# Kernel optimization log

Measured on AMD Instinct MI355X. Metric: run time of the kernel, lower is better.

The kernel has to match this reference:

```python
import jax, jax.numpy as jnp
import numpy as np

N_TOKEN = 1024
N_I = 512
VOCAB = 10
D = 1024
L = 12
H_MLP = 4096
EPS = 1e-5  # torch LayerNorm default
B = 8


def layer_norm(x, g, b):
    mu = jnp.mean(x, axis=-1, keepdims=True)
    var = jnp.mean(jnp.square(x - mu), axis=-1, keepdims=True)
    return (x - mu) * jax.lax.rsqrt(var + EPS) * g + b


def setup_inputs() -> dict:
    key = jax.random.key(0)
    ks = jax.random.split(key, 12)
    s = 0.02  # init scale for weights
    return {
        'xt': jax.random.randint(ks[0], (B, N_TOKEN - N_I), 0, VOCAB),
        'zi': jax.random.randint(ks[1], (B, N_I), 0, VOCAB),
        'pos_emb': jax.random.normal(ks[2], (N_TOKEN, D), jnp.float32) * s,
        't_emb': jax.random.normal(ks[3], (VOCAB, D), jnp.float32) * s,
        'Wq': jax.random.normal(ks[4], (L, D, D), jnp.float32) * s,
        'Wk': jax.random.normal(ks[5], (L, D, D), jnp.float32) * s,
        'Wv': jax.random.normal(ks[6], (L, D, D), jnp.float32) * s,
        'ln1_g': jnp.ones((L, D), jnp.float32),
        'ln1_b': jnp.zeros((L, D), jnp.float32),
        'ln2_g': jnp.ones((L, D), jnp.float32),
        'ln2_b': jnp.zeros((L, D), jnp.float32),
        'mlp_w1': jax.random.normal(ks[7], (L, D, H_MLP), jnp.float32) * s,
        'mlp_b1': jnp.zeros((L, H_MLP), jnp.float32),
        'mlp_w2': jax.random.normal(ks[8], (L, H_MLP, D), jnp.float32) * s,
        'mlp_b2': jnp.zeros((L, D), jnp.float32),
        'ro_w': jax.random.normal(ks[9], (D, 1), jnp.float32) * s,
        'ro_b': jnp.zeros((1,), jnp.float32),
    }


def _forward(xt, zi, pos_emb, t_emb, Wq, Wk, Wv, ln1_g, ln1_b, ln2_g, ln2_b,
             mlp_w1, mlp_b1, mlp_w2, mlp_b2, ro_w, ro_b):
    # token embeddings: image tokens get -(c - zi)^2/2 in the first VOCAB dims, 0 elsewhere
    opts = jnp.arange(VOCAB, dtype=jnp.float32)
    leave = -jnp.square(opts[None, None, :] - zi[:, :, None].astype(jnp.float32)) * 0.5  # [B, N_I, V]
    emb_i = jnp.pad(leave, ((0, 0), (0, 0), (0, D - VOCAB)))  # [B, N_I, D]
    emb_t = t_emb[xt]                                          # [B, T1, D]
    H = jnp.concatenate([emb_i, emb_t], axis=1) + pos_emb[None, :, :]  # [B, T, D]

    inv_sqrt_d = np.float32(1.0 / np.sqrt(D))

    def step(H, p):
        wq, wk, wv, g1, b1, g2, b2, w1, bb1, w2, bb2 = p
        H1 = layer_norm(H, g1, b1)
        q = H1 @ wq
        k = H1 @ wk
        v = H1 @ wv
        attn = jnp.einsum('bid,bjd->bij', q, k) * inv_sqrt_d  # [B, T, T]
        attn = jax.nn.softmax(attn, axis=-1)
        H = H + jnp.einsum('bij,bjd->bid', attn, v)
        H2 = layer_norm(H, g2, b2)
        # torch nn.GELU default is exact (erf) gelu
        H = H + (jax.nn.gelu(H2 @ w1 + bb1, approximate=False) @ w2 + bb2)
        return H, None

    H, _ = jax.lax.scan(step, H, (Wq, Wk, Wv, ln1_g, ln1_b, ln2_g, ln2_b,
                                  mlp_w1, mlp_b1, mlp_w2, mlp_b2))
    pred = H @ ro_w + ro_b  # [B, T, 1]
    return pred[:, :N_I, 0]  # [B, N_I]


def reference(xt, zi, pos_emb, t_emb, Wq, Wk, Wv, ln1_g, ln1_b, ln2_g, ln2_b,
              mlp_w1, mlp_b1, mlp_w2, mlp_b2, ro_w, ro_b):
    return _forward(xt, zi, pos_emb, t_emb, Wq, Wk, Wv, ln1_g, ln1_b, ln2_g, ln2_b,
                    mlp_w1, mlp_b1, mlp_w2, mlp_b2, ro_w, ro_b)
```

## Files before the change

kernel.cpp:

```cpp
#include <hip/hip_runtime.h>
#include <cstdint>
#include <cmath>

typedef unsigned short u16;
typedef unsigned int u32;
typedef short bf16x8 __attribute__((ext_vector_type(8)));
typedef float f32x4 __attribute__((ext_vector_type(4)));

#define DEV static __device__ __forceinline__

DEV u16 f2bf(float f) {
  union { float f; u32 u; } v; v.f = f;
  return (u16)((v.u + 0x7FFFu + ((v.u >> 16) & 1u)) >> 16);
}
DEV float bf2f(u32 lo16) {
  union { u32 u; float f; } v; v.u = lo16 << 16; return v.f;
}

DEV void gload16(const void* g, u16* l) {
  __builtin_amdgcn_global_load_lds(
      (const __attribute__((address_space(1))) void*)g,
      (__attribute__((address_space(3))) void*)l, 16, 0, 0);
}

template<int MODE>
__global__ __launch_bounds__(512, 4)
void gemm8(const u16* __restrict__ A, const u16* __restrict__ Bt,
           void* __restrict__ Cv, const float* __restrict__ bias,
           u16* __restrict__ Vt, int M, int N, int K, int ldA, int ldB,
           float scale)
{
  __shared__ __align__(16) u16 As[128 * 64];
  __shared__ __align__(16) u16 Bs[128 * 64];

  const long m0 = (long)blockIdx.x * 128, n0 = (long)blockIdx.y * 128;
  const int t = threadIdx.x;
  const int wave = t >> 6, lane = t & 63;
  const int wr = (wave >> 2) * 64, wc = (wave & 3) * 32;
  const int lg = lane >> 4, lr = lane & 15;

  const long ldA2 = (long)ldA * 2, ldB2 = (long)ldB * 2;

  const int rl = lane >> 3, c7 = lane & 7;
  const int sb = (c7 * 16) ^ (rl << 4);
  const char* aP[2]; const char* bP[2];
  u16* aL[2]; u16* bL[2];
  {
    const char* Ab = (const char*)A;
    const char* Bb = (const char*)Bt;
    #pragma unroll
    for (int c = 0; c < 2; ++c) {
      const int q = c * 8 + wave;
      aP[c] = Ab + (m0 + q * 8 + rl) * ldA2 + sb;
      bP[c] = Bb + (n0 + q * 8 + rl) * ldB2 + sb;
      aL[c] = As + q * 512;
      bL[c] = Bs + q * 512;
    }
  }

  const int rswz = (lr & 7) << 4;
  auto rd = [&](const u16* base, int row, int cbyte) -> bf16x8 {
    return *reinterpret_cast<const bf16x8*>(
        reinterpret_cast<const char*>(base) + row * 128 + (cbyte ^ rswz));
  };

  f32x4 acc[4][2];
  #pragma unroll
  for (int i = 0; i < 4; ++i)
    #pragma unroll
    for (int j = 0; j < 2; ++j)
      acc[i][j] = (f32x4){0.f, 0.f, 0.f, 0.f};

  for (int k0 = 0; k0 < K; k0 += 64) {
    #pragma unroll
    for (int c = 0; c < 2; ++c) {
      gload16(aP[c], aL[c]);
      gload16(bP[c], bL[c]);
      aP[c] += 128; bP[c] += 128;
    }
    __syncthreads();

    #pragma unroll
    for (int ks = 0; ks < 2; ++ks) {
      bf16x8 a[4], b[2];
      #pragma unroll
      for (int i = 0; i < 4; ++i)
        a[i] = rd(As, wr + i * 16 + lr, ks * 64 + lg * 16);
      #pragma unroll
      for (int i = 0; i < 2; ++i)
        b[i] = rd(Bs, wc + i * 16 + lr, ks * 64 + lg * 16);
      #pragma unroll
      for (int mi = 0; mi < 4; ++mi)
        #pragma unroll
        for (int ni = 0; ni < 2; ++ni)
          acc[mi][ni] = __builtin_amdgcn_mfma_f32_16x16x32_bf16(a[mi], b[ni], acc[mi][ni], 0, 0, 0);
    }
    __syncthreads();
  }

  #pragma unroll
  for (int mi = 0; mi < 4; ++mi) {
    #pragma unroll
    for (int ni = 0; ni < 2; ++ni) {
      #pragma unroll
      for (int r = 0; r < 4; ++r) {
        const long grow = m0 + wr + mi * 16 + lg * 4 + r;
        const long gcol = n0 + wc + ni * 16 + lr;
        const float v = acc[mi][ni][r];
        if constexpr (MODE == 3) {
          const float x = v + bias[gcol];
          const float u2 = 1.59576912f * x * (1.f + 0.044715f * x * x);
          const float ge = x / (1.f + __expf(-u2));
          ((u16*)Cv)[grow * N + gcol] = f2bf(ge);
        } else if constexpr (MODE == 4) {
          float* Cp = (float*)Cv;
          const long idx = grow * N + gcol;
          Cp[idx] = Cp[idx] + v + bias[gcol];
        } else if constexpr (MODE == 5) {
          if (gcol < 2048) {
            ((u16*)Cv)[grow * 2048 + gcol] = f2bf(v * scale);
          } else {
            const long b = grow >> 10, tk = grow & 1023, d = gcol - 2048;
            Vt[(b << 20) + (d << 10) + tk] = f2bf(v);
          }
        }
      }
    }
  }
}

template<int MODE>
__global__ __launch_bounds__(512, 4)
void gemm8b(const u16* __restrict__ A, const u16* __restrict__ Bt,
            void* __restrict__ Cv, int N, int K, int ldA, int ldB,
            long sA, long sB, long sC, float scale)
{
  __shared__ __align__(16) u16 As[128 * 64];
  __shared__ __align__(16) u16 Bs[128 * 64];

  const int bz = blockIdx.z;
  const long m0 = (long)blockIdx.x * 128, n0 = (long)blockIdx.y * 128;
  const int t = threadIdx.x;
  const int wave = t >> 6, lane = t & 63;
  const int wr = (wave >> 2) * 64, wc = (wave & 3) * 32;
  const int lg = lane >> 4, lr = lane & 15;

  const long ldA2 = (long)ldA * 2, ldB2 = (long)ldB * 2;

  const int rl = lane >> 3, c7 = lane & 7;
  const int sb = (c7 * 16) ^ (rl << 4);
  const char* aP[2]; const char* bP[2];
  u16* aL[2]; u16* bL[2];
  {
    const char* Ab = (const char*)(A + (long)bz * sA);
    const char* Bb = (const char*)(Bt + (long)bz * sB);
    #pragma unroll
    for (int c = 0; c < 2; ++c) {
      const int q = c * 8 + wave;
      aP[c] = Ab + (m0 + q * 8 + rl) * ldA2 + sb;
      bP[c] = Bb + (n0 + q * 8 + rl) * ldB2 + sb;
      aL[c] = As + q * 512;
      bL[c] = Bs + q * 512;
    }
  }

  const int rswz = (lr & 7) << 4;
  auto rd = [&](const u16* base, int row, int cbyte) -> bf16x8 {
    return *reinterpret_cast<const bf16x8*>(
        reinterpret_cast<const char*>(base) + row * 128 + (cbyte ^ rswz));
  };

  f32x4 acc[4][2];
  #pragma unroll
  for (int i = 0; i < 4; ++i)
    #pragma unroll
    for (int j = 0; j < 2; ++j)
      acc[i][j] = (f32x4){0.f, 0.f, 0.f, 0.f};

  for (int k0 = 0; k0 < K; k0 += 64) {
    #pragma unroll
    for (int c = 0; c < 2; ++c) {
      gload16(aP[c], aL[c]);
      gload16(bP[c], bL[c]);
      aP[c] += 128; bP[c] += 128;
    }
    __syncthreads();

    #pragma unroll
    for (int ks = 0; ks < 2; ++ks) {
      bf16x8 a[4], b[2];
      #pragma unroll
      for (int i = 0; i < 4; ++i)
        a[i] = rd(As, wr + i * 16 + lr, ks * 64 + lg * 16);
      #pragma unroll
      for (int i = 0; i < 2; ++i)
        b[i] = rd(Bs, wc + i * 16 + lr, ks * 64 + lg * 16);
      #pragma unroll
      for (int mi = 0; mi < 4; ++mi)
        #pragma unroll
        for (int ni = 0; ni < 2; ++ni)
          acc[mi][ni] = __builtin_amdgcn_mfma_f32_16x16x32_bf16(a[mi], b[ni], acc[mi][ni], 0, 0, 0);
    }
    __syncthreads();
  }

  #pragma unroll
  for (int mi = 0; mi < 4; ++mi) {
    #pragma unroll
    for (int ni = 0; ni < 2; ++ni) {
      #pragma unroll
      for (int r = 0; r < 4; ++r) {
        const long grow = m0 + wr + mi * 16 + lg * 4 + r;
        const long gcol = n0 + wc + ni * 16 + lr;
        const float v = acc[mi][ni][r];
        if constexpr (MODE == 0) {
          u16* Cp = (u16*)Cv + (long)bz * sC;
          Cp[grow * N + gcol] = f2bf(v * scale);
        } else if constexpr (MODE == 2) {
          float* Cp = (float*)Cv + (long)bz * sC;
          Cp[grow * N + gcol] += v;
        }
      }
    }
  }
}

__global__ __launch_bounds__(256)
void trans_k(const float* __restrict__ wq, const float* __restrict__ wk,
             const float* __restrict__ wv, const float* __restrict__ w1,
             const float* __restrict__ w2, u16* __restrict__ ob)
{
  __shared__ u16 T[64][68];
  const int b = blockIdx.x;
  const float* in; u16* out; int K, N, tk, tn;
  if (b < 768) {
    const int m = b >> 8, tt = b & 255;
    in = (m == 0) ? wq : (m == 1) ? wk : wv;
    out = ob + (long)m * 1048576L;
    K = 1024; N = 1024; tk = tt >> 4; tn = tt & 15;
  } else if (b < 1792) {
    const int tt = b - 768;
    in = w1; out = ob + 3L * 1048576L; K = 1024; N = 4096;
    tk = tt >> 6; tn = tt & 63;
  } else {
    const int tt = b - 1792;
    in = w2; out = ob + 7L * 1048576L; K = 4096; N = 1024;
    tk = tt >> 4; tn = tt & 15;
  }
  const int k0 = tk * 64, n0 = tn * 64;
  const int t = threadIdx.x;
  {
    const int r = t >> 2, cq = (t & 3) * 16;
    const float* src = in + (long)(k0 + r) * N + n0 + cq;
    #pragma unroll
    for (int q = 0; q < 4; ++q) {
      const float4 v = *reinterpret_cast<const float4*>(src + q * 4);
      T[r][cq + q * 4 + 0] = f2bf(v.x);
      T[r][cq + q * 4 + 1] = f2bf(v.y);
      T[r][cq + q * 4 + 2] = f2bf(v.z);
      T[r][cq + q * 4 + 3] = f2bf(v.w);
    }
  }
  __syncthreads();
  {
    const int n = t >> 2, kq2 = (t & 3) * 16;
    u16 tmp[16];
    #pragma unroll
    for (int j = 0; j < 16; ++j) tmp[j] = T[kq2 + j][n];
    uint4* dst = reinterpret_cast<uint4*>(out + (long)(n0 + n) * K + k0 + kq2);
    dst[0] = *reinterpret_cast<const uint4*>(&tmp[0]);
    dst[1] = *reinterpret_cast<const uint4*>(&tmp[8]);
  }
}

__global__ __launch_bounds__(256)
void embed_k(const int* __restrict__ xt, const int* __restrict__ zi,
             const float* __restrict__ pos, const float* __restrict__ temb,
             float* __restrict__ H)
{
  const int bt = blockIdx.x;
  const int b = bt >> 10, tk = bt & 1023;
  const int d = threadIdx.x * 4;
  const float4 p = reinterpret_cast<const float4*>(pos + (long)tk * 1024)[threadIdx.x];
  float4 v;
  if (tk < 512) {
    const float z = (float)zi[b * 512 + tk];
    const float c0 = (float)(d + 0) - z, c1 = (float)(d + 1) - z;
    const float c2 = (float)(d + 2) - z, c3 = (float)(d + 3) - z;
    v.x = (d + 0 < 10) ? -0.5f * c0 * c0 : 0.f;
    v.y = (d + 1 < 10) ? -0.5f * c1 * c1 : 0.f;
    v.z = (d + 2 < 10) ? -0.5f * c2 * c2 : 0.f;
    v.w = (d + 3 < 10) ? -0.5f * c3 * c3 : 0.f;
  } else {
    const float* te = temb + (long)xt[b * 512 + (tk - 512)] * 1024;
    v = reinterpret_cast<const float4*>(te)[threadIdx.x];
  }
  float4 o; o.x = v.x + p.x; o.y = v.y + p.y; o.z = v.z + p.z; o.w = v.w + p.w;
  reinterpret_cast<float4*>(H + (long)bt * 1024)[threadIdx.x] = o;
}

__global__ __launch_bounds__(256)
void ln_k(const float* __restrict__ X, const float* __restrict__ g,
          const float* __restrict__ bta, u16* __restrict__ Y)
{
  __shared__ float sm[8];
  const long row = blockIdx.x;
  const float4 x = reinterpret_cast<const float4*>(X + row * 1024)[threadIdx.x];
  float s1 = x.x + x.y + x.z + x.w;
  float s2 = x.x * x.x + x.y * x.y + x.z * x.z + x.w * x.w;
  #pragma unroll
  for (int o = 32; o > 0; o >>= 1) { s1 += __shfl_down(s1, o); s2 += __shfl_down(s2, o); }
  const int w = threadIdx.x >> 6, ln = threadIdx.x & 63;
  if (ln == 0) { sm[w] = s1; sm[4 + w] = s2; }
  __syncthreads();
  s1 = sm[0] + sm[1] + sm[2] + sm[3];
  s2 = sm[4] + sm[5] + sm[6] + sm[7];
  const float mu = s1 * (1.f / 1024.f);
  const float var = s2 * (1.f / 1024.f) - mu * mu;
  const float inv = rsqrtf(var + 1e-5f);
  const float4 gg = reinterpret_cast<const float4*>(g)[threadIdx.x];
  const float4 bb = reinterpret_cast<const float4*>(bta)[threadIdx.x];
  const u32 o0 = (u32)f2bf((x.x - mu) * inv * gg.x + bb.x) | ((u32)f2bf((x.y - mu) * inv * gg.y + bb.y) << 16);
  const u32 o1 = (u32)f2bf((x.z - mu) * inv * gg.z + bb.z) | ((u32)f2bf((x.w - mu) * inv * gg.w + bb.w) << 16);
  reinterpret_cast<uint2*>(Y + row * 1024)[threadIdx.x] = make_uint2(o0, o1);
}

__global__ __launch_bounds__(256)
void sm_k(const u16* __restrict__ S, u16* __restrict__ P)
{
  __shared__ float sm[8];
  const long row = blockIdx.x;
  const uint2 raw = reinterpret_cast<const uint2*>(S + row * 1024)[threadIdx.x];
  const float x0 = bf2f(raw.x & 0xffffu), x1 = bf2f(raw.x >> 16);
  const float x2 = bf2f(raw.y & 0xffffu), x3 = bf2f(raw.y >> 16);
  float m = fmaxf(fmaxf(x0, x1), fmaxf(x2, x3));
  #pragma unroll
  for (int o = 32; o > 0; o >>= 1) m = fmaxf(m, __shfl_down(m, o));
  const int w = threadIdx.x >> 6, ln = threadIdx.x & 63;
  if (ln == 0) sm[w] = m;
  __syncthreads();
  m = fmaxf(fmaxf(sm[0], sm[1]), fmaxf(sm[2], sm[3]));
  const float e0 = __expf(x0 - m), e1 = __expf(x1 - m);
  const float e2 = __expf(x2 - m), e3 = __expf(x3 - m);
  float s = e0 + e1 + e2 + e3;
  #pragma unroll
  for (int o = 32; o > 0; o >>= 1) s += __shfl_down(s, o);
  if (ln == 0) sm[4 + w] = s;
  __syncthreads();
  const float tot = sm[4] + sm[5] + sm[6] + sm[7];
  const float r = 1.0f / tot;
  const u32 o0 = (u32)f2bf(e0 * r) | ((u32)f2bf(e1 * r) << 16);
  const u32 o1 = (u32)f2bf(e2 * r) | ((u32)f2bf(e3 * r) << 16);
  reinterpret_cast<uint2*>(P + row * 1024)[threadIdx.x] = make_uint2(o0, o1);
}

__global__ __launch_bounds__(256)
void ro_k(const float* __restrict__ H, const float* __restrict__ w,
          const float* __restrict__ b, float* __restrict__ out)
{
  __shared__ float sm[4];
  const int row = blockIdx.x;
  const int bb = row >> 9, i = row & 511;
  const float* h = H + ((long)bb * 1024 + i) * 1024;
  const float4 x = reinterpret_cast<const float4*>(h)[threadIdx.x];
  const float4 ww = reinterpret_cast<const float4*>(w)[threadIdx.x];
  float s = x.x * ww.x + x.y * ww.y + x.z * ww.z + x.w * ww.w;
  #pragma unroll
  for (int o = 32; o > 0; o >>= 1) s += __shfl_down(s, o);
  const int wv = threadIdx.x >> 6, ln = threadIdx.x & 63;
  if (ln == 0) sm[wv] = s;
  __syncthreads();
  if (threadIdx.x == 0) out[row] = sm[0] + sm[1] + sm[2] + sm[3] + b[0];
}

extern "C" void kernel_launch(void* const* d_in, const int* in_sizes, int n_in,
                              void* d_out, int out_size, void* d_ws, size_t ws_size,
                              hipStream_t stream)
{
  const int* xt = (const int*)d_in[0];
  const int* zi = (const int*)d_in[1];
  const float* pos  = (const float*)d_in[2];
  const float* temb = (const float*)d_in[3];
  const float* Wq = (const float*)d_in[4];
  const float* Wk = (const float*)d_in[5];
  const float* Wv = (const float*)d_in[6];
  const float* ln1g = (const float*)d_in[7];
  const float* ln1b = (const float*)d_in[8];
  const float* ln2g = (const float*)d_in[9];
  const float* ln2b = (const float*)d_in[10];
  const float* w1 = (const float*)d_in[11];
  const float* b1 = (const float*)d_in[12];
  const float* w2 = (const float*)d_in[13];
  const float* b2 = (const float*)d_in[14];
  const float* row_w = (const float*)d_in[15];
  const float* row_b = (const float*)d_in[16];

  char* ws = (char*)d_ws;
  const long MB = 1024 * 1024;
  float* H   = (float*)(ws + 0);
  u16*   H1  = (u16*)(ws + 32 * MB);
  u16*   QK  = (u16*)(ws + 48 * MB);
  u16*   Vt  = (u16*)(ws + 80 * MB);
  u16*   S   = (u16*)(ws + 96 * MB);
  u16*   P   = (u16*)(ws + 112 * MB);
  u16*   G   = (u16*)(ws + 80 * MB);
  u16*   WT  = (u16*)(ws + 144 * MB);

  u16* W1T = WT + 3 * 1048576L;
  u16* W2T = WT + 7 * 1048576L;

  const long s1M = 1024L * 1024L;
  const long s2M = 2L * 1024L * 1024L;

  embed_k<<<8192, 256, 0, stream>>>(xt, zi, pos, temb, H);

  for (int l = 0; l < 12; ++l) {
    const float* wq = Wq + (long)l * s1M;
    const float* wk = Wk + (long)l * s1M;
    const float* wv = Wv + (long)l * s1M;
    const float* mw1 = w1 + (long)l * 1024L * 4096L;
    const float* mb1 = b1 + (long)l * 4096L;
    const float* mw2 = w2 + (long)l * 4096L * 1024L;
    const float* mb2 = b2 + (long)l * 1024L;

    trans_k<<<2816, 256, 0, stream>>>(wq, wk, wv, mw1, mw2, WT);

    ln_k<<<8192, 256, 0, stream>>>(H, ln1g + l * 1024, ln1b + l * 1024, H1);

    gemm8<5><<<dim3(64, 24, 1), 512, 0, stream>>>(H1, WT, QK, nullptr, Vt,
        8192, 3072, 1024, 1024, 1024, 1.f);

    gemm8b<0><<<dim3(8, 8, 8), 512, 0, stream>>>(QK, QK + 1024, S,
        1024, 1024, 2048, 2048, s2M, s2M, s1M, 1.f / 32.f);

    sm_k<<<8192, 256, 0, stream>>>(S, P);

    gemm8b<2><<<dim3(8, 8, 8), 512, 0, stream>>>(P, Vt, (void*)H,
        1024, 1024, 1024, 1024, s1M, s1M, s1M, 1.f);

    ln_k<<<8192, 256, 0, stream>>>(H, ln2g + l * 1024, ln2b + l * 1024, H1);

    gemm8<3><<<dim3(64, 32, 1), 512, 0, stream>>>(H1, W1T, G, mb1, nullptr,
        8192, 4096, 1024, 1024, 1024, 1.f);
    gemm8<4><<<dim3(64, 8, 1), 512, 0, stream>>>(G, W2T, (void*)H, mb2, nullptr,
        8192, 1024, 4096, 4096, 4096, 1.f);
  }

  ro_k<<<4096, 256, 0, stream>>>(H, row_w, row_b, (float*)d_out);
}
```

Before: 3.768 ms.

## Double-buffer LDS tiles in GEMM kernels to overlap loads with MFMA

Both GEMM kernels now keep two LDS buffers and issue the global-to-LDS loads for the next K tile before computing on the current one, with one barrier per iteration instead of two. This is meant to hide global load latency behind the matrix-core work. In exchange, LDS use per block doubles to 64KB, which may reduce how many blocks fit per CU. There is also a correctness risk, because the next stage is written into the buffer that other waves may still be reading from the previous iteration.

```diff
diff --git a/kernel.cpp b/kernel.cpp
--- a/kernel.cpp
+++ b/kernel.cpp
@@ -30,8 +30,8 @@
            u16* __restrict__ Vt, int M, int N, int K, int ldA, int ldB,
            float scale)
 {
-  __shared__ __align__(16) u16 As[128 * 64];
-  __shared__ __align__(16) u16 Bs[128 * 64];
+  __shared__ __align__(16) u16 As[2 * 128 * 64];
+  __shared__ __align__(16) u16 Bs[2 * 128 * 64];
 
   const long m0 = (long)blockIdx.x * 128, n0 = (long)blockIdx.y * 128;
   const int t = threadIdx.x;
@@ -44,7 +44,6 @@
   const int rl = lane >> 3, c7 = lane & 7;
   const int sb = (c7 * 16) ^ (rl << 4);
   const char* aP[2]; const char* bP[2];
-  u16* aL[2]; u16* bL[2];
   {
     const char* Ab = (const char*)A;
     const char* Bb = (const char*)Bt;
@@ -53,10 +52,18 @@
       const int q = c * 8 + wave;
       aP[c] = Ab + (m0 + q * 8 + rl) * ldA2 + sb;
       bP[c] = Bb + (n0 + q * 8 + rl) * ldB2 + sb;
-      aL[c] = As + q * 512;
-      bL[c] = Bs + q * 512;
-    }
-  }
+    }
+  }
+
+  auto stage = [&](int buf) {
+    #pragma unroll
+    for (int c = 0; c < 2; ++c) {
+      const int q = c * 8 + wave;
+      gload16(aP[c], As + buf * 8192 + q * 512);
+      gload16(bP[c], Bs + buf * 8192 + q * 512);
+      aP[c] += 128; bP[c] += 128;
+    }
+  };
 
   const int rswz = (lr & 7) << 4;
   auto rd = [&](const u16* base, int row, int cbyte) -> bf16x8 {
@@ -71,31 +78,39 @@
     for (int j = 0; j < 2; ++j)
       acc[i][j] = (f32x4){0.f, 0.f, 0.f, 0.f};
 
-  for (int k0 = 0; k0 < K; k0 += 64) {
-    #pragma unroll
-    for (int c = 0; c < 2; ++c) {
-      gload16(aP[c], aL[c]);
-      gload16(bP[c], bL[c]);
-      aP[c] += 128; bP[c] += 128;
-    }
-    __syncthreads();
-
+  const int NT = K >> 6;
+
+  stage(0);
+  asm volatile("s_waitcnt vmcnt(0)" ::: "memory");
+  __builtin_amdgcn_s_barrier();
+
+  for (int tt = 0; tt < NT; ++tt) {
+    const int cur = tt & 1;
+    const bool more = (tt + 1 < NT);
+    if (more) stage(cur ^ 1);
+
+    const u16* Ab = As + cur * 8192;
+    const u16* Bb = Bs + cur * 8192;
     #pragma unroll
     for (int ks = 0; ks < 2; ++ks) {
       bf16x8 a[4], b[2];
       #pragma unroll
       for (int i = 0; i < 4; ++i)
-        a[i] = rd(As, wr + i * 16 + lr, ks * 64 + lg * 16);
+        a[i] = rd(Ab, wr + i * 16 + lr, ks * 64 + lg * 16);
       #pragma unroll
       for (int i = 0; i < 2; ++i)
-        b[i] = rd(Bs, wc + i * 16 + lr, ks * 64 + lg * 16);
+        b[i] = rd(Bb, wc + i * 16 + lr, ks * 64 + lg * 16);
       #pragma unroll
       for (int mi = 0; mi < 4; ++mi)
         #pragma unroll
         for (int ni = 0; ni < 2; ++ni)
           acc[mi][ni] = __builtin_amdgcn_mfma_f32_16x16x32_bf16(a[mi], b[ni], acc[mi][ni], 0, 0, 0);
     }
-    __syncthreads();
+
+    if (more) {
+      asm volatile("s_waitcnt vmcnt(0)" ::: "memory");
+      __builtin_amdgcn_s_barrier();
+    }
   }
 
   #pragma unroll
@@ -135,8 +150,8 @@
             void* __restrict__ Cv, int N, int K, int ldA, int ldB,
             long sA, long sB, long sC, float scale)
 {
-  __shared__ __align__(16) u16 As[128 * 64];
-  __shared__ __align__(16) u16 Bs[128 * 64];
+  __shared__ __align__(16) u16 As[2 * 128 * 64];
+  __shared__ __align__(16) u16 Bs[2 * 128 * 64];
 
   const int bz = blockIdx.z;
   const long m0 = (long)blockIdx.x * 128, n0 = (long)blockIdx.y * 128;
@@ -150,7 +165,6 @@
   const int rl = lane >> 3, c7 = lane & 7;
   const int sb = (c7 * 16) ^ (rl << 4);
   const char* aP[2]; const char* bP[2];
-  u16* aL[2]; u16* bL[2];
   {
     const char* Ab = (const char*)(A + (long)bz * sA);
     const char* Bb = (const char*)(Bt + (long)bz * sB);
@@ -159,10 +173,18 @@
       const int q = c * 8 + wave;
       aP[c] = Ab + (m0 + q * 8 + rl) * ldA2 + sb;
       bP[c] = Bb + (n0 + q * 8 + rl) * ldB2 + sb;
-      aL[c] = As + q * 512;
-      bL[c] = Bs + q * 512;
-    }
-  }
+    }
+  }
+
+  auto stage = [&](int buf) {
+    #pragma unroll
+    for (int c = 0; c < 2; ++c) {
+      const int q = c * 8 + wave;
+      gload16(aP[c], As + buf * 8192 + q * 512);
+      gload16(bP[c], Bs + buf * 8192 + q * 512);
+      aP[c] += 128; bP[c] += 128;
+    }
+  };
 
   const int rswz = (lr & 7) << 4;
   auto rd = [&](const u16* base, int row, int cbyte) -> bf16x8 {
@@ -177,31 +199,39 @@
     for (int j = 0; j < 2; ++j)
       acc[i][j] = (f32x4){0.f, 0.f, 0.f, 0.f};
 
-  for (int k0 = 0; k0 < K; k0 += 64) {
-    #pragma unroll
-    for (int c = 0; c < 2; ++c) {
-      gload16(aP[c], aL[c]);
-      gload16(bP[c], bL[c]);
-      aP[c] += 128; bP[c] += 128;
-    }
-    __syncthreads();
-
+  const int NT = K >> 6;
+
+  stage(0);
+  asm volatile("s_waitcnt vmcnt(0)" ::: "memory");
+  __builtin_amdgcn_s_barrier();
+
+  for (int tt = 0; tt < NT; ++tt) {
+    const int cur = tt & 1;
+    const bool more = (tt + 1 < NT);
+    if (more) stage(cur ^ 1);
+
+    const u16* Ab = As + cur * 8192;
+    const u16* Bb = Bs + cur * 8192;
     #pragma unroll
     for (int ks = 0; ks < 2; ++ks) {
       bf16x8 a[4], b[2];
       #pragma unroll
       for (int i = 0; i < 4; ++i)
-        a[i] = rd(As, wr + i * 16 + lr, ks * 64 + lg * 16);
+        a[i] = rd(Ab, wr + i * 16 + lr, ks * 64 + lg * 16);
       #pragma unroll
       for (int i = 0; i < 2; ++i)
-        b[i] = rd(Bs, wc + i * 16 + lr, ks * 64 + lg * 16);
+        b[i] = rd(Bb, wc + i * 16 + lr, ks * 64 + lg * 16);
       #pragma unroll
       for (int mi = 0; mi < 4; ++mi)
         #pragma unroll
         for (int ni = 0; ni < 2; ++ni)
           acc[mi][ni] = __builtin_amdgcn_mfma_f32_16x16x32_bf16(a[mi], b[ni], acc[mi][ni], 0, 0, 0);
     }
-    __syncthreads();
+
+    if (more) {
+      asm volatile("s_waitcnt vmcnt(0)" ::: "memory");
+      __builtin_amdgcn_s_barrier();
+    }
   }
 
   #pragma unroll
```

Result: slower. 3.936 ms (+4.5%).
